# Performance work log

Hardware: AMD Instinct MI355X
Metric: run time of the kernel (lower is better)

The kernel has to match this reference:

```python
import jax, jax.numpy as jnp
import numpy as np

B, S, H, NH = 2, 2048, 1024, 16
P = H // NH

def setup_inputs() -> dict:
    key = jax.random.key(0)
    k1, k2, k3, k4 = jax.random.split(key, 4)
    x = jax.random.normal(k1, (B, S, H), dtype=jnp.float32)
    mask = jax.random.randint(k2, (B, S), 0, 2).astype(jnp.int32)
    # weights: (num_heads, 3, hidden, partial) -- the leading singleton dim of the
    # torch parameter is pure broadcast, dropped here.
    W = jax.random.normal(k3, (NH, 3, H, P), dtype=jnp.float32) * (1.0 / np.sqrt(H))
    Wl = jax.random.normal(k4, (H, H), dtype=jnp.float32) * (1.0 / np.sqrt(H))
    bl = jnp.zeros((H,), dtype=jnp.float32)
    return {"x": x, "mask": mask, "W": W, "Wl": Wl, "bl": bl}

def reference(x, mask, W, Wl, bl):
    nh, _, h, p = W.shape
    scale = 1.0 / np.sqrt(p)
    # kvq[b, t, n, s, p]; t=0 keys, t=1 values, t=2 queries (unbind order in source)
    kvq = jnp.einsum('bsh,nthp->btnsp', x, W)
    keys, values, queries = kvq[:, 0], kvq[:, 1], kvq[:, 2]  # each [B, NH, S, P]
    # NOTE: source computes keys @ queries^T -> scores[b,n,i,j] = k_i . q_j
    scores = jnp.einsum('bnip,bnjp->bnij', keys, queries) * scale
    # mask==0 zeroes out the LAST axis (query positions), exactly as the fancy-index write
    scores = jnp.where(mask[:, None, None, :] == 0, jnp.float32(-1e12), scores)
    # softmax over dim=2 (key axis), as in the source (Softmax(dim=2))
    w = jax.nn.softmax(scores, axis=2)
    out = jnp.einsum('bnij,bnjp->bnip', w, values)  # [B, NH, S, P]
    b, _, s, _ = out.shape
    hidden = out.transpose(0, 2, 1, 3).reshape(b, s, nh * p)  # concat heads
    return hidden @ Wl.T + bl
```

## Files before the change

kernel.cpp:

```cpp
#include <hip/hip_runtime.h>

#define B_ 2
#define S_ 2048
#define H_ 1024
#define NH_ 16
#define P_ 64

using f32x4 = __attribute__((ext_vector_type(4))) float;
using i32x4 = __attribute__((ext_vector_type(4))) int;
using f16   = _Float16;
using f16x8 = __attribute__((ext_vector_type(8))) f16;
using f16x4 = __attribute__((ext_vector_type(4))) f16;

#define QSCALE 0.18033688f

static __device__ __forceinline__ f16x8 ldh8(const f16* p) { return *(const f16x8*)p; }
static __device__ __forceinline__ f32x4 ld4f(const float* p) { return *(const f32x4*)p; }

static __device__ __forceinline__ f32x4 mm16(f16x8 a, f16x8 b, f32x4 c) {
  return __builtin_amdgcn_mfma_f32_16x16x32_f16(a, b, c, 0, 0, 0);
}

__global__ __launch_bounds__(256) void tw_kernel(
    const float* __restrict__ W, f16* __restrict__ WtH)
{
  __shared__ float T[64 * 65];
  const int tid = threadIdx.x;
  const int nt = blockIdx.x >> 4;
  const int h0 = (blockIdx.x & 15) * 64;
  const float* src = W + (size_t)nt * H_ * P_ + (size_t)h0 * P_;
  #pragma unroll
  for (int r = 0; r < 4; ++r) {
    int idx = tid + r * 256;
    int h = idx >> 4, p4 = (idx & 15) << 2;
    f32x4 v = ld4f(src + (size_t)h * P_ + p4);
    #pragma unroll
    for (int i = 0; i < 4; ++i) T[(p4 + i) * 65 + h] = v[i];
  }
  __syncthreads();
  f16* dh = WtH + (size_t)nt * P_ * H_;
  #pragma unroll
  for (int r = 0; r < 4; ++r) {
    int idx = tid + r * 256;
    int p = idx >> 4, h4 = (idx & 15) << 2;
    f16x4 hv;
    #pragma unroll
    for (int i = 0; i < 4; ++i) hv[i] = (f16)T[p * 65 + h4 + i];
    *(f16x4*)(dh + (size_t)p * H_ + h0 + h4) = hv;
  }
}

__global__ __launch_bounds__(256) void swl_kernel(
    const float* __restrict__ Wl, f16* __restrict__ WlH)
{
  int idx = blockIdx.x * 256 + threadIdx.x;
  f32x4 v = ((const f32x4*)Wl)[idx];
  f16x4 h;
  #pragma unroll
  for (int i = 0; i < 4; ++i) h[i] = (f16)v[i];
  ((f16x4*)WlH)[idx] = h;
}

__global__ __launch_bounds__(256) void qkv_kernel(
    const float* __restrict__ x, const f16* __restrict__ WtH,
    f16* __restrict__ Kh, f16* __restrict__ Qh, f16* __restrict__ VTh)
{
  __shared__ f16 xls[2][64 * 64];

  int blk = blockIdx.x;
  const int st = blk & 31; blk >>= 5;
  const int n = blk & 15;
  const int b = blk >> 4;
  const int s0 = st * 64;
  const int tid = threadIdx.x;
  const int w = tid >> 6, lane = tid & 63, q = lane >> 4, fr = lane & 15;
  const int bn = b * NH_ + n;

  const int srow = tid >> 2, scc = tid & 3;
  const float* xsrc = x + ((size_t)b * S_ + s0 + srow) * H_ + 16 * scc;
  const int c0 = ((2 * scc) ^ (srow & 7)) * 8;
  const int c1 = ((2 * scc + 1) ^ (srow & 7)) * 8;

  auto stage = [&](int k0, int bs) {
    f32x4 v0 = ld4f(xsrc + k0),     v1 = ld4f(xsrc + k0 + 4);
    f32x4 v2 = ld4f(xsrc + k0 + 8), v3 = ld4f(xsrc + k0 + 12);
    f16x8 a, b2;
    #pragma unroll
    for (int e = 0; e < 4; ++e) {
      a[e] = (f16)v0[e];  a[e + 4] = (f16)v1[e];
      b2[e] = (f16)v2[e]; b2[e + 4] = (f16)v3[e];
    }
    *(f16x8*)&xls[bs][srow * 64 + c0] = a;
    *(f16x8*)&xls[bs][srow * 64 + c1] = b2;
  };

  const f16* WtK = WtH + ((size_t)(n * 3 + 0) * P_ + 16 * w + fr) * H_ + 8 * q;
  const f16* WtV = WtH + ((size_t)(n * 3 + 1) * P_ + 16 * w + fr) * H_ + 8 * q;
  const f16* WtQ = WtH + ((size_t)(n * 3 + 2) * P_ + 16 * w + fr) * H_ + 8 * q;

  f32x4 accK[4] = {}, accQ[4] = {}, accV[4] = {};

  stage(0, 0);
  for (int step = 0; step < 16; ++step) {
    __syncthreads();
    if (step < 15) stage((step + 1) * 64, (step + 1) & 1);
    const int bs = step & 1;
    const int k0 = step * 64;

    f16x8 xf[4][2];
    #pragma unroll
    for (int ss = 0; ss < 4; ++ss) {
      int row = 16 * ss + fr;
      #pragma unroll
      for (int ks = 0; ks < 2; ++ks) {
        int ch = ((q + 4 * ks) ^ (row & 7)) * 8;
        xf[ss][ks] = *(const f16x8*)&xls[bs][row * 64 + ch];
      }
    }
    f16x8 wk0 = ldh8(WtK + k0), wk1 = ldh8(WtK + k0 + 32);
    f16x8 wq0 = ldh8(WtQ + k0), wq1 = ldh8(WtQ + k0 + 32);
    f16x8 wv0 = ldh8(WtV + k0), wv1 = ldh8(WtV + k0 + 32);
    #pragma unroll
    for (int ss = 0; ss < 4; ++ss) {
      accK[ss] = mm16(wk0, xf[ss][0], accK[ss]);
      accK[ss] = mm16(wk1, xf[ss][1], accK[ss]);
      accQ[ss] = mm16(wq0, xf[ss][0], accQ[ss]);
      accQ[ss] = mm16(wq1, xf[ss][1], accQ[ss]);
      accV[ss] = mm16(xf[ss][0], wv0, accV[ss]);
      accV[ss] = mm16(xf[ss][1], wv1, accV[ss]);
    }
  }

  #pragma unroll
  for (int ss = 0; ss < 4; ++ss) {
    f16x4 hK, hQ;
    #pragma unroll
    for (int c = 0; c < 4; ++c) {
      hK[c] = (f16)accK[ss][c];
      hQ[c] = (f16)(accQ[ss][c] * QSCALE);
    }
    size_t off = ((size_t)bn * S_ + (s0 + 16 * ss + fr)) * P_ + 16 * w + 4 * q;
    *(f16x4*)(Kh + off) = hK;
    *(f16x4*)(Qh + off) = hQ;
  }
  #pragma unroll
  for (int ss = 0; ss < 4; ++ss) {
    f16x4 hV;
    #pragma unroll
    for (int c = 0; c < 4; ++c) hV[c] = (f16)accV[ss][c];
    size_t off = ((size_t)bn * P_ + (16 * w + fr)) * S_ + s0 + 16 * ss + 4 * q;
    *(f16x4*)(VTh + off) = hV;
  }
}

__global__ __launch_bounds__(256) void stats_kernel(
    const f16* __restrict__ Kh, const f16* __restrict__ Qh,
    float* __restrict__ csuminv)
{
  __shared__ float zbuf[2 * 128];
  const int tid = threadIdx.x;
  const int bid = blockIdx.x;
  const int j0 = (bid & 15) * 128;
  const int bn = bid >> 4;
  const int w = tid >> 6, lane = tid & 63, q = lane >> 4, fr = lane & 15;
  const int jb = 64 * (w & 1), ih = w >> 1, ib0 = 32 * ih;

  f16x8 qf[4][2];
  #pragma unroll
  for (int jt = 0; jt < 4; ++jt)
    #pragma unroll
    for (int ks = 0; ks < 2; ++ks)
      qf[jt][ks] = ldh8(Qh + ((size_t)bn * S_ + (j0 + jb + 16 * jt + fr)) * P_ + 8 * q + 32 * ks);

  f32x4 z[4] = {};
  f16x8 kA[2][2], kB[2][2];

  auto loadK = [&](f16x8 (&kf)[2][2], int i0) {
    #pragma unroll
    for (int it = 0; it < 2; ++it)
      #pragma unroll
      for (int ks = 0; ks < 2; ++ks)
        kf[it][ks] = ldh8(Kh + ((size_t)bn * S_ + (i0 + ib0 + 16 * it + fr)) * P_ + 8 * q + 32 * ks);
  };
  auto step = [&](f16x8 (&kf)[2][2]) {
    f32x4 sc[4][2] = {};
    __builtin_amdgcn_s_setprio(1);
    #pragma unroll
    for (int ks = 0; ks < 2; ++ks)
      #pragma unroll
      for (int jt = 0; jt < 4; ++jt)
        #pragma unroll
        for (int it = 0; it < 2; ++it)
          sc[jt][it] = mm16(qf[jt][ks], kf[it][ks], sc[jt][it]);
    __builtin_amdgcn_s_setprio(0);
    #pragma unroll
    for (int jt = 0; jt < 4; ++jt)
      #pragma unroll
      for (int c = 0; c < 4; ++c)
        z[jt][c] += exp2f(sc[jt][0][c]) + exp2f(sc[jt][1][c]);
  };

  loadK(kA, 0);
  for (int i0 = 0; i0 < S_; i0 += 128) {
    loadK(kB, i0 + 64);
    step(kA);
    loadK(kA, (i0 + 128) & (S_ - 1));
    step(kB);
  }

  #pragma unroll
  for (int msk = 1; msk <= 8; msk <<= 1)
    #pragma unroll
    for (int jt = 0; jt < 4; ++jt)
      #pragma unroll
      for (int c = 0; c < 4; ++c)
        z[jt][c] += __shfl_xor(z[jt][c], msk, 64);

  if (fr == 0) {
    #pragma unroll
    for (int jt = 0; jt < 4; ++jt)
      *(f32x4*)&zbuf[ih * 128 + jb + 16 * jt + 4 * q] = z[jt];
  }
  __syncthreads();
  if (tid < 128)
    csuminv[(size_t)bn * S_ + j0 + tid] = 1.0f / (zbuf[tid] + zbuf[128 + tid]);
}

__global__ __launch_bounds__(256) void scale_kernel(
    f16* __restrict__ VT, const float* __restrict__ csuminv,
    const int* __restrict__ mask, float* __restrict__ Cbuf)
{
  const int bid = blockIdx.x;
  const int bn = bid >> 4;
  const int b = bn >> 4;
  const int p = (bid & 15) * 4 + (threadIdx.x >> 6);
  const int lane = threadIdx.x & 63;
  f16* row = VT + ((size_t)bn * P_ + p) * S_;
  const float* zr = csuminv + (size_t)bn * S_;
  const int* mr = mask + (size_t)b * S_;
  float acc = 0.0f;
  #pragma unroll
  for (int k = 0; k < 4; ++k) {
    int s = (lane + 64 * k) * 8;
    f16x8 v = *(const f16x8*)(row + s);
    f32x4 z0 = ld4f(zr + s), z1 = ld4f(zr + s + 4);
    i32x4 m0 = *(const i32x4*)(mr + s), m1 = *(const i32x4*)(mr + s + 4);
    f16x8 o;
    #pragma unroll
    for (int e = 0; e < 4; ++e) {
      float fv = (float)v[e];
      if (m0[e] != 0) o[e] = (f16)(fv * z0[e]);
      else { o[e] = (f16)0.0f; acc += fv; }
      float fv2 = (float)v[e + 4];
      if (m1[e] != 0) o[e + 4] = (f16)(fv2 * z1[e]);
      else { o[e + 4] = (f16)0.0f; acc += fv2; }
    }
    *(f16x8*)(row + s) = o;
  }
  #pragma unroll
  for (int msk = 1; msk <= 32; msk <<= 1) acc += __shfl_xor(acc, msk, 64);
  if (lane == 0) Cbuf[bn * P_ + p] = acc * (1.0f / S_);
}

__global__ __launch_bounds__(256) void av_kernel(
    const f16* __restrict__ Kh, const f16* __restrict__ Qh,
    const f16* __restrict__ VT, const float* __restrict__ Cbuf,
    f16* __restrict__ hidh)
{
  __shared__ f16  elds[4][64 * 40];
  __shared__ float accl[64 * 68];
  const int tid = threadIdx.x;
  const int bid = blockIdx.x;
  const int i0 = (bid & 31) * 64;
  const int bn = bid >> 5;
  const int b = bn >> 4, n = bn & 15;
  const int w = tid >> 6, lane = tid & 63, q = lane >> 4, fr = lane & 15;
  f16* ew = &elds[w][0];

  f16x8 kf[4][2];
  #pragma unroll
  for (int it = 0; it < 4; ++it)
    #pragma unroll
    for (int ks = 0; ks < 2; ++ks)
      kf[it][ks] = ldh8(Kh + ((size_t)bn * S_ + (i0 + 16 * it + fr)) * P_ + 8 * q + 32 * ks);

  f32x4 opv[4][4] = {};

  f16x8 aqA[2][2], vaA[4], aqB[2][2], vaB[4];

  auto loadQ = [&](f16x8 (&aq)[2][2], f16x8 (&va)[4], int T) {
    const int j0 = T * 128 + w * 32;
    #pragma unroll
    for (int jt = 0; jt < 2; ++jt)
      #pragma unroll
      for (int ks = 0; ks < 2; ++ks)
        aq[jt][ks] = ldh8(Qh + ((size_t)bn * S_ + (j0 + 16 * jt + fr)) * P_ + 8 * q + 32 * ks);
    #pragma unroll
    for (int pt = 0; pt < 4; ++pt)
      va[pt] = ldh8(VT + ((size_t)bn * P_ + (16 * pt + fr)) * S_ + j0 + 8 * q);
  };

  auto compute = [&](f16x8 (&aq)[2][2], f16x8 (&va)[4]) {
    #pragma unroll
    for (int it = 0; it < 4; ++it) {
      f32x4 s0 = {}, s1 = {};
      __builtin_amdgcn_s_setprio(1);
      s0 = mm16(aq[0][0], kf[it][0], s0);
      s0 = mm16(aq[0][1], kf[it][1], s0);
      s1 = mm16(aq[1][0], kf[it][0], s1);
      s1 = mm16(aq[1][1], kf[it][1], s1);
      __builtin_amdgcn_s_setprio(0);
      f16x4 e0, e1;
      #pragma unroll
      for (int c = 0; c < 4; ++c) {
        e0[c] = (f16)exp2f(s0[c]);
        e1[c] = (f16)exp2f(s1[c]);
      }
      *(f16x4*)(ew + (16 * it + fr) * 40 + 4 * q)      = e0;
      *(f16x4*)(ew + (16 * it + fr) * 40 + 16 + 4 * q) = e1;
    }
    __builtin_amdgcn_s_setprio(1);
    #pragma unroll
    for (int it = 0; it < 4; ++it) {
      f16x8 ef = *(const f16x8*)(ew + (16 * it + fr) * 40 + 8 * q);
      #pragma unroll
      for (int pt = 0; pt < 4; ++pt)
        opv[pt][it] = mm16(va[pt], ef, opv[pt][it]);
    }
    __builtin_amdgcn_s_setprio(0);
  };

  loadQ(aqA, vaA, 0);
  for (int T = 0; T < 16; T += 2) {
    loadQ(aqB, vaB, T + 1);
    compute(aqA, vaA);
    loadQ(aqA, vaA, (T + 2) & 15);
    compute(aqB, vaB);
  }

  #pragma unroll
  for (int r = 0; r < 4; ++r) {
    __syncthreads();
    if (w == r) {
      #pragma unroll
      for (int it = 0; it < 4; ++it)
        #pragma unroll
        for (int pt = 0; pt < 4; ++pt) {
          float* a = &accl[(16 * it + fr) * 68 + 16 * pt + 4 * q];
          if (r == 0) *(f32x4*)a = opv[pt][it];
          else {
            f32x4 old = *(const f32x4*)a;
            #pragma unroll
            for (int c = 0; c < 4; ++c) old[c] += opv[pt][it][c];
            *(f32x4*)a = old;
          }
        }
    }
  }
  __syncthreads();

  const int ti = tid >> 2;
  const int tp = (tid & 3) << 4;
  const float* cb = Cbuf + bn * P_ + tp;
  f16* dst = hidh + ((size_t)b * S_ + (i0 + ti)) * H_ + n * P_ + tp;
  #pragma unroll
  for (int h = 0; h < 2; ++h) {
    f32x4 a0 = *(const f32x4*)&accl[ti * 68 + tp + 8 * h];
    f32x4 a1 = *(const f32x4*)&accl[ti * 68 + tp + 8 * h + 4];
    f32x4 c0 = ld4f(cb + 8 * h);
    f32x4 c1 = ld4f(cb + 8 * h + 4);
    f16x8 o;
    #pragma unroll
    for (int e = 0; e < 4; ++e) {
      o[e]     = (f16)(a0[e] + c0[e]);
      o[e + 4] = (f16)(a1[e] + c1[e]);
    }
    *(f16x8*)(dst + 8 * h) = o;
  }
}

__global__ __launch_bounds__(256) void final_kernel(
    const f16* __restrict__ hidh, const f16* __restrict__ WlH,
    const float* __restrict__ bl, float* __restrict__ out)
{
  __shared__ f16 hl[2][64 * 64];
  const int tid = threadIdx.x;
  const int ot = blockIdx.x & 15;
  const int rt = blockIdx.x >> 4;
  const int r0 = rt * 64, o0 = ot * 64;
  const int w = tid >> 6, lane = tid & 63, q = lane >> 4, fr = lane & 15;

  const int srow = tid >> 2, scc = tid & 3;
  const f16* hsrc = hidh + (size_t)(r0 + srow) * H_ + 16 * scc;
  const int c0 = ((2 * scc) ^ (srow & 7)) * 8;
  const int c1 = ((2 * scc + 1) ^ (srow & 7)) * 8;

  auto stage = [&](int k0, int bs) {
    f16x8 a = ldh8(hsrc + k0);
    f16x8 b2 = ldh8(hsrc + k0 + 8);
    *(f16x8*)&hl[bs][srow * 64 + c0] = a;
    *(f16x8*)&hl[bs][srow * 64 + c1] = b2;
  };

  const f16* WlA = WlH + ((size_t)(o0 + 16 * w + fr)) * H_ + 8 * q;

  f32x4 acc[4] = {};

  stage(0, 0);
  for (int step = 0; step < 16; ++step) {
    __syncthreads();
    if (step < 15) stage((step + 1) * 64, (step + 1) & 1);
    const int bs = step & 1;
    const int k0 = step * 64;

    f16x8 bh[4][2];
    #pragma unroll
    for (int ss = 0; ss < 4; ++ss) {
      int row = 16 * ss + fr;
      #pragma unroll
      for (int ks = 0; ks < 2; ++ks) {
        int ch = ((q + 4 * ks) ^ (row & 7)) * 8;
        bh[ss][ks] = *(const f16x8*)&hl[bs][row * 64 + ch];
      }
    }
    f16x8 ah0 = ldh8(WlA + k0);
    f16x8 ah1 = ldh8(WlA + k0 + 32);
    #pragma unroll
    for (int ss = 0; ss < 4; ++ss) {
      acc[ss] = mm16(ah0, bh[ss][0], acc[ss]);
      acc[ss] = mm16(ah1, bh[ss][1], acc[ss]);
    }
  }

  const int o = o0 + 16 * w + 4 * q;
  f32x4 bv = ld4f(bl + o);
  #pragma unroll
  for (int ss = 0; ss < 4; ++ss) {
    f32x4 v;
    #pragma unroll
    for (int c = 0; c < 4; ++c) v[c] = acc[ss][c] + bv[c];
    *(f32x4*)(out + (size_t)(r0 + 16 * ss + fr) * H_ + o) = v;
  }
}

extern "C" void kernel_launch(void* const* d_in, const int* in_sizes, int n_in,
                              void* d_out, int out_size, void* d_ws, size_t ws_size,
                              hipStream_t stream) {
  const float* x    = (const float*)d_in[0];
  const int*   mask = (const int*)d_in[1];
  const float* W    = (const float*)d_in[2];
  const float* Wl   = (const float*)d_in[3];
  const float* bl   = (const float*)d_in[4];
  float* out = (float*)d_out;

  const size_t SZ  = (size_t)B_ * NH_ * S_ * P_;
  const size_t SZW = (size_t)NH_ * 3 * H_ * P_;
  const size_t SZL = (size_t)H_ * H_;
  const size_t SZC = (size_t)B_ * NH_ * S_;
  const size_t SZH = (size_t)B_ * S_ * H_;

  char* p = (char*)d_ws;
  f16*   Kh   = (f16*)p;  p += SZ * 2;
  f16*   Qh   = (f16*)p;  p += SZ * 2;
  f16*   VTh  = (f16*)p;  p += SZ * 2;
  f16*   WtH  = (f16*)p;  p += SZW * 2;
  f16*   WlH  = (f16*)p;  p += SZL * 2;
  f16*   hidh = (f16*)p;  p += SZH * 2;
  float* csuminv = (float*)p; p += SZC * 4;
  float* Cbuf    = (float*)p; p += (size_t)B_ * NH_ * P_ * 4;

  tw_kernel   <<<NH_ * 3 * (H_ / 64), 256, 0, stream>>>(W, WtH);
  swl_kernel  <<<(SZL / 4) / 256, 256, 0, stream>>>(Wl, WlH);
  qkv_kernel  <<<B_ * NH_ * (S_ / 64), 256, 0, stream>>>(x, WtH, Kh, Qh, VTh);
  stats_kernel<<<B_ * NH_ * (S_ / 128), 256, 0, stream>>>(Kh, Qh, csuminv);
  scale_kernel<<<B_ * NH_ * 16, 256, 0, stream>>>(VTh, csuminv, mask, Cbuf);
  av_kernel   <<<B_ * NH_ * (S_ / 64), 256, 0, stream>>>(
      Kh, Qh, VTh, Cbuf, hidh);
  final_kernel<<<(B_ * S_ / 64) * (H_ / 64), 256, 0, stream>>>(
      hidh, WlH, bl, out);
}
```

Measured before the change: 218.7 us.

## Split attention over query halves into two partials plus reduce kernel

```diff
diff --git a/kernel.cpp b/kernel.cpp
--- a/kernel.cpp
+++ b/kernel.cpp
@@ -11,6 +11,7 @@
 using f16   = _Float16;
 using f16x8 = __attribute__((ext_vector_type(8))) f16;
 using f16x4 = __attribute__((ext_vector_type(4))) f16;
+using h16x2 = __attribute__((ext_vector_type(2))) __fp16;
 
 #define QSCALE 0.18033688f
 
@@ -264,18 +265,17 @@
 
 __global__ __launch_bounds__(256) void av_kernel(
     const f16* __restrict__ Kh, const f16* __restrict__ Qh,
-    const f16* __restrict__ VT, const float* __restrict__ Cbuf,
-    f16* __restrict__ hidh)
-{
-  __shared__ f16  elds[4][64 * 40];
-  __shared__ float accl[64 * 68];
+    const f16* __restrict__ VT, f16* __restrict__ Up0, f16* __restrict__ Up1)
+{
+  __shared__ __align__(16) char smem[18432];
   const int tid = threadIdx.x;
   const int bid = blockIdx.x;
-  const int i0 = (bid & 31) * 64;
-  const int bn = bid >> 5;
+  const int jh = bid & 1;
+  const int i0 = ((bid >> 1) & 31) * 64;
+  const int bn = bid >> 6;
   const int b = bn >> 4, n = bn & 15;
   const int w = tid >> 6, lane = tid & 63, q = lane >> 4, fr = lane & 15;
-  f16* ew = &elds[w][0];
+  f16* ew = (f16*)smem + w * (64 * 36);
 
   f16x8 kf[4][2];
   #pragma unroll
@@ -286,58 +286,46 @@
 
   f32x4 opv[4][4] = {};
 
-  f16x8 aqA[2][2], vaA[4], aqB[2][2], vaB[4];
-
-  auto loadQ = [&](f16x8 (&aq)[2][2], f16x8 (&va)[4], int T) {
-    const int j0 = T * 128 + w * 32;
+  for (int T = 0; T < 8; ++T) {
+    const int j0 = jh * 1024 + T * 128 + w * 32;
+
+    f16x8 aq[2][2];
     #pragma unroll
     for (int jt = 0; jt < 2; ++jt)
       #pragma unroll
       for (int ks = 0; ks < 2; ++ks)
         aq[jt][ks] = ldh8(Qh + ((size_t)bn * S_ + (j0 + 16 * jt + fr)) * P_ + 8 * q + 32 * ks);
+    f16x8 va[4];
     #pragma unroll
     for (int pt = 0; pt < 4; ++pt)
       va[pt] = ldh8(VT + ((size_t)bn * P_ + (16 * pt + fr)) * S_ + j0 + 8 * q);
-  };
-
-  auto compute = [&](f16x8 (&aq)[2][2], f16x8 (&va)[4]) {
+
     #pragma unroll
     for (int it = 0; it < 4; ++it) {
       f32x4 s0 = {}, s1 = {};
-      __builtin_amdgcn_s_setprio(1);
       s0 = mm16(aq[0][0], kf[it][0], s0);
       s0 = mm16(aq[0][1], kf[it][1], s0);
       s1 = mm16(aq[1][0], kf[it][0], s1);
       s1 = mm16(aq[1][1], kf[it][1], s1);
-      __builtin_amdgcn_s_setprio(0);
-      f16x4 e0, e1;
-      #pragma unroll
-      for (int c = 0; c < 4; ++c) {
-        e0[c] = (f16)exp2f(s0[c]);
-        e1[c] = (f16)exp2f(s1[c]);
-      }
-      *(f16x4*)(ew + (16 * it + fr) * 40 + 4 * q)      = e0;
-      *(f16x4*)(ew + (16 * it + fr) * 40 + 16 + 4 * q) = e1;
-    }
-    __builtin_amdgcn_s_setprio(1);
+      union { f16x4 v; h16x2 h[2]; } e0, e1;
+      e0.h[0] = __builtin_amdgcn_cvt_pkrtz(exp2f(s0[0]), exp2f(s0[1]));
+      e0.h[1] = __builtin_amdgcn_cvt_pkrtz(exp2f(s0[2]), exp2f(s0[3]));
+      e1.h[0] = __builtin_amdgcn_cvt_pkrtz(exp2f(s1[0]), exp2f(s1[1]));
+      e1.h[1] = __builtin_amdgcn_cvt_pkrtz(exp2f(s1[2]), exp2f(s1[3]));
+      *(f16x4*)(ew + (16 * it + fr) * 36 + 4 * q)      = e0.v;
+      *(f16x4*)(ew + (16 * it + fr) * 36 + 16 + 4 * q) = e1.v;
+    }
+
     #pragma unroll
     for (int it = 0; it < 4; ++it) {
-      f16x8 ef = *(const f16x8*)(ew + (16 * it + fr) * 40 + 8 * q);
+      f16x8 ef = *(const f16x8*)(ew + (16 * it + fr) * 36 + 8 * q);
       #pragma unroll
       for (int pt = 0; pt < 4; ++pt)
         opv[pt][it] = mm16(va[pt], ef, opv[pt][it]);
     }
-    __builtin_amdgcn_s_setprio(0);
-  };
-
-  loadQ(aqA, vaA, 0);
-  for (int T = 0; T < 16; T += 2) {
-    loadQ(aqB, vaB, T + 1);
-    compute(aqA, vaA);
-    loadQ(aqA, vaA, (T + 2) & 15);
-    compute(aqB, vaB);
-  }
-
+  }
+
+  float* accl = (float*)smem;
   #pragma unroll
   for (int r = 0; r < 4; ++r) {
     __syncthreads();
@@ -359,24 +347,44 @@
   }
   __syncthreads();
 
+  f16* Up = jh ? Up1 : Up0;
   const int ti = tid >> 2;
   const int tp = (tid & 3) << 4;
-  const float* cb = Cbuf + bn * P_ + tp;
-  f16* dst = hidh + ((size_t)b * S_ + (i0 + ti)) * H_ + n * P_ + tp;
+  f16* dst = Up + ((size_t)b * S_ + (i0 + ti)) * H_ + n * P_ + tp;
   #pragma unroll
   for (int h = 0; h < 2; ++h) {
     f32x4 a0 = *(const f32x4*)&accl[ti * 68 + tp + 8 * h];
     f32x4 a1 = *(const f32x4*)&accl[ti * 68 + tp + 8 * h + 4];
-    f32x4 c0 = ld4f(cb + 8 * h);
-    f32x4 c1 = ld4f(cb + 8 * h + 4);
     f16x8 o;
     #pragma unroll
     for (int e = 0; e < 4; ++e) {
-      o[e]     = (f16)(a0[e] + c0[e]);
-      o[e + 4] = (f16)(a1[e] + c1[e]);
+      o[e]     = (f16)a0[e];
+      o[e + 4] = (f16)a1[e];
     }
     *(f16x8*)(dst + 8 * h) = o;
   }
+}
+
+__global__ __launch_bounds__(256) void reduce_kernel(
+    const f16* __restrict__ Up0, const f16* __restrict__ Up1,
+    const float* __restrict__ Cbuf, f16* __restrict__ hidh)
+{
+  size_t flat = ((size_t)blockIdx.x * 256 + threadIdx.x) * 8;
+  const int h = (int)(flat & (H_ - 1));
+  const int b = (int)(flat >> 21);
+  const int n = h >> 6;
+  const int bn = b * NH_ + n;
+  f16x8 u0 = ldh8(Up0 + flat);
+  f16x8 u1 = ldh8(Up1 + flat);
+  f32x4 c0 = ld4f(Cbuf + bn * P_ + (h & 63));
+  f32x4 c1 = ld4f(Cbuf + bn * P_ + (h & 63) + 4);
+  f16x8 o;
+  #pragma unroll
+  for (int e = 0; e < 4; ++e) {
+    o[e]     = (f16)((float)u0[e] + (float)u1[e] + c0[e]);
+    o[e + 4] = (f16)((float)u0[e + 4] + (float)u1[e + 4] + c1[e]);
+  }
+  *(f16x8*)(hidh + flat) = o;
 }
 
 __global__ __launch_bounds__(256) void final_kernel(
@@ -466,16 +474,20 @@
   f16*   WtH  = (f16*)p;  p += SZW * 2;
   f16*   WlH  = (f16*)p;  p += SZL * 2;
   f16*   hidh = (f16*)p;  p += SZH * 2;
+  f16*   Up0  = (f16*)p;  p += SZH * 2;
+  f16*   Up1  = (f16*)p;  p += SZH * 2;
   float* csuminv = (float*)p; p += SZC * 4;
   float* Cbuf    = (float*)p; p += (size_t)B_ * NH_ * P_ * 4;
 
-  tw_kernel   <<<NH_ * 3 * (H_ / 64), 256, 0, stream>>>(W, WtH);
-  swl_kernel  <<<(SZL / 4) / 256, 256, 0, stream>>>(Wl, WlH);
-  qkv_kernel  <<<B_ * NH_ * (S_ / 64), 256, 0, stream>>>(x, WtH, Kh, Qh, VTh);
-  stats_kernel<<<B_ * NH_ * (S_ / 128), 256, 0, stream>>>(Kh, Qh, csuminv);
-  scale_kernel<<<B_ * NH_ * 16, 256, 0, stream>>>(VTh, csuminv, mask, Cbuf);
-  av_kernel   <<<B_ * NH_ * (S_ / 64), 256, 0, stream>>>(
-      Kh, Qh, VTh, Cbuf, hidh);
-  final_kernel<<<(B_ * S_ / 64) * (H_ / 64), 256, 0, stream>>>(
+  tw_kernel    <<<NH_ * 3 * (H_ / 64), 256, 0, stream>>>(W, WtH);
+  swl_kernel   <<<(SZL / 4) / 256, 256, 0, stream>>>(Wl, WlH);
+  qkv_kernel   <<<B_ * NH_ * (S_ / 64), 256, 0, stream>>>(x, WtH, Kh, Qh, VTh);
+  stats_kernel <<<B_ * NH_ * (S_ / 128), 256, 0, stream>>>(Kh, Qh, csuminv);
+  scale_kernel <<<B_ * NH_ * 16, 256, 0, stream>>>(VTh, csuminv, mask, Cbuf);
+  av_kernel    <<<B_ * NH_ * (S_ / 64) * 2, 256, 0, stream>>>(
+      Kh, Qh, VTh, Up0, Up1);
+  reduce_kernel<<<(int)(SZH / (256 * 8)), 256, 0, stream>>>(
+      Up0, Up1, Cbuf, hidh);
+  final_kernel <<<(B_ * S_ / 64) * (H_ / 64), 256, 0, stream>>>(
       hidh, WlH, bl, out);
 }
```

After: 224.2 us. 1.03x slower.

## Simplify av_kernel loop, shrink LDS, use packed f16 conversion

Applied to the files above, without the earlier changes.

```diff
diff --git a/kernel.cpp b/kernel.cpp
--- a/kernel.cpp
+++ b/kernel.cpp
@@ -11,6 +11,7 @@
 using f16   = _Float16;
 using f16x8 = __attribute__((ext_vector_type(8))) f16;
 using f16x4 = __attribute__((ext_vector_type(4))) f16;
+using h16x2 = __attribute__((ext_vector_type(2))) __fp16;
 
 #define QSCALE 0.18033688f
 
@@ -267,15 +268,14 @@
     const f16* __restrict__ VT, const float* __restrict__ Cbuf,
     f16* __restrict__ hidh)
 {
-  __shared__ f16  elds[4][64 * 40];
-  __shared__ float accl[64 * 68];
+  __shared__ __align__(16) char smem[18432];
   const int tid = threadIdx.x;
   const int bid = blockIdx.x;
   const int i0 = (bid & 31) * 64;
   const int bn = bid >> 5;
   const int b = bn >> 4, n = bn & 15;
   const int w = tid >> 6, lane = tid & 63, q = lane >> 4, fr = lane & 15;
-  f16* ew = &elds[w][0];
+  f16* ew = (f16*)smem + w * (64 * 36);
 
   f16x8 kf[4][2];
   #pragma unroll
@@ -284,60 +284,50 @@
     for (int ks = 0; ks < 2; ++ks)
       kf[it][ks] = ldh8(Kh + ((size_t)bn * S_ + (i0 + 16 * it + fr)) * P_ + 8 * q + 32 * ks);
 
+  const f16* qp  = Qh + ((size_t)bn * S_ + (w * 32 + fr)) * P_ + 8 * q;
+  const f16* vp0 = VT + ((size_t)bn * P_ + fr) * S_ + w * 32 + 8 * q;
+  const f16* vp1 = vp0 + (size_t)16 * S_;
+  const f16* vp2 = vp0 + (size_t)32 * S_;
+  const f16* vp3 = vp0 + (size_t)48 * S_;
+
   f32x4 opv[4][4] = {};
 
-  f16x8 aqA[2][2], vaA[4], aqB[2][2], vaB[4];
-
-  auto loadQ = [&](f16x8 (&aq)[2][2], f16x8 (&va)[4], int T) {
-    const int j0 = T * 128 + w * 32;
-    #pragma unroll
-    for (int jt = 0; jt < 2; ++jt)
-      #pragma unroll
-      for (int ks = 0; ks < 2; ++ks)
-        aq[jt][ks] = ldh8(Qh + ((size_t)bn * S_ + (j0 + 16 * jt + fr)) * P_ + 8 * q + 32 * ks);
-    #pragma unroll
-    for (int pt = 0; pt < 4; ++pt)
-      va[pt] = ldh8(VT + ((size_t)bn * P_ + (16 * pt + fr)) * S_ + j0 + 8 * q);
-  };
-
-  auto compute = [&](f16x8 (&aq)[2][2], f16x8 (&va)[4]) {
+  for (int T = 0; T < 16; ++T) {
+    f16x8 aq00 = ldh8(qp);
+    f16x8 aq01 = ldh8(qp + 32);
+    f16x8 aq10 = ldh8(qp + 1024);
+    f16x8 aq11 = ldh8(qp + 1056);
+    f16x8 va0 = ldh8(vp0), va1 = ldh8(vp1), va2 = ldh8(vp2), va3 = ldh8(vp3);
+    qp += 128 * 64;
+    vp0 += 128; vp1 += 128; vp2 += 128; vp3 += 128;
+
     #pragma unroll
     for (int it = 0; it < 4; ++it) {
       f32x4 s0 = {}, s1 = {};
-      __builtin_amdgcn_s_setprio(1);
-      s0 = mm16(aq[0][0], kf[it][0], s0);
-      s0 = mm16(aq[0][1], kf[it][1], s0);
-      s1 = mm16(aq[1][0], kf[it][0], s1);
-      s1 = mm16(aq[1][1], kf[it][1], s1);
-      __builtin_amdgcn_s_setprio(0);
-      f16x4 e0, e1;
-      #pragma unroll
-      for (int c = 0; c < 4; ++c) {
-        e0[c] = (f16)exp2f(s0[c]);
-        e1[c] = (f16)exp2f(s1[c]);
-      }
-      *(f16x4*)(ew + (16 * it + fr) * 40 + 4 * q)      = e0;
-      *(f16x4*)(ew + (16 * it + fr) * 40 + 16 + 4 * q) = e1;
-    }
-    __builtin_amdgcn_s_setprio(1);
+      s0 = mm16(aq00, kf[it][0], s0);
+      s0 = mm16(aq01, kf[it][1], s0);
+      s1 = mm16(aq10, kf[it][0], s1);
+      s1 = mm16(aq11, kf[it][1], s1);
+      union { f16x4 v; h16x2 h[2]; } e0, e1;
+      e0.h[0] = __builtin_amdgcn_cvt_pkrtz(exp2f(s0[0]), exp2f(s0[1]));
+      e0.h[1] = __builtin_amdgcn_cvt_pkrtz(exp2f(s0[2]), exp2f(s0[3]));
+      e1.h[0] = __builtin_amdgcn_cvt_pkrtz(exp2f(s1[0]), exp2f(s1[1]));
+      e1.h[1] = __builtin_amdgcn_cvt_pkrtz(exp2f(s1[2]), exp2f(s1[3]));
+      *(f16x4*)(ew + (16 * it + fr) * 36 + 4 * q)      = e0.v;
+      *(f16x4*)(ew + (16 * it + fr) * 36 + 16 + 4 * q) = e1.v;
+    }
+
     #pragma unroll
     for (int it = 0; it < 4; ++it) {
-      f16x8 ef = *(const f16x8*)(ew + (16 * it + fr) * 40 + 8 * q);
-      #pragma unroll
-      for (int pt = 0; pt < 4; ++pt)
-        opv[pt][it] = mm16(va[pt], ef, opv[pt][it]);
-    }
-    __builtin_amdgcn_s_setprio(0);
-  };
-
-  loadQ(aqA, vaA, 0);
-  for (int T = 0; T < 16; T += 2) {
-    loadQ(aqB, vaB, T + 1);
-    compute(aqA, vaA);
-    loadQ(aqA, vaA, (T + 2) & 15);
-    compute(aqB, vaB);
-  }
-
+      f16x8 ef = *(const f16x8*)(ew + (16 * it + fr) * 36 + 8 * q);
+      opv[0][it] = mm16(va0, ef, opv[0][it]);
+      opv[1][it] = mm16(va1, ef, opv[1][it]);
+      opv[2][it] = mm16(va2, ef, opv[2][it]);
+      opv[3][it] = mm16(va3, ef, opv[3][it]);
+    }
+  }
+
+  float* accl = (float*)smem;
   #pragma unroll
   for (int r = 0; r < 4; ++r) {
     __syncthreads();
```

Result: no change. 218.6 us (-0.0%).
